# Optimization experiments

Measured on AMD Instinct MI355X. Metric: run time of the kernel, lower is better.

The kernel has to match this reference:

```python
import jax, jax.numpy as jnp
import numpy as np

B, S, H, NH = 2, 2048, 1024, 16
HD = H // NH

def setup_inputs() -> dict:
    key = jax.random.key(0)
    ks = jax.random.split(key, 11)
    scale = 1.0 / np.sqrt(H)
    inp = {
        "query": jax.random.normal(ks[0], (B, S, H), jnp.float32),
        "key": jax.random.normal(ks[1], (B, S, H), jnp.float32),
        "value": jax.random.normal(ks[2], (B, S, H), jnp.float32),
        "mask": jnp.ones((B, 1, S, S), jnp.int32),
        "Wq": jax.random.normal(ks[3], (H, H), jnp.float32) * scale,
        "bq": jnp.zeros((H,), jnp.float32),
        "Wk": jax.random.normal(ks[4], (H, H), jnp.float32) * scale,
        "bk": jnp.zeros((H,), jnp.float32),
        "Wv": jax.random.normal(ks[5], (H, H), jnp.float32) * scale,
        "bv": jnp.zeros((H,), jnp.float32),
        "Wo": jax.random.normal(ks[6], (H, H), jnp.float32) * scale,
        "bo": jnp.zeros((H,), jnp.float32),
    }
    return inp

def reference(query, key, value, mask, Wq, bq, Wk, bk, Wv, bv, Wo, bo):
    b = query.shape[0]
    # Linear projections (torch Linear: x @ W.T + b)
    Q = query @ Wq.T + bq
    K = key @ Wk.T + bk
    V = value @ Wv.T + bv
    # [b, s, h] -> [b, nh, s, hd]
    Q = Q.reshape(b, -1, NH, HD).transpose(0, 2, 1, 3)
    K = K.reshape(b, -1, NH, HD).transpose(0, 2, 1, 3)
    V = V.reshape(b, -1, NH, HD).transpose(0, 2, 1, 3)
    scores = jnp.einsum('bhid,bhjd->bhij', Q, K) / np.sqrt(HD)
    scores = jnp.where(mask == 0, jnp.float32(-1e9), scores)
    attn_weights = jax.nn.softmax(scores, axis=-1)
    # dropout = 0.0 (eval mode) -> identity
    context = jnp.einsum('bhij,bhjd->bhid', attn_weights, V)
    context = context.transpose(0, 2, 1, 3).reshape(b, -1, H)
    output = context @ Wo.T + bo
    return (output, attn_weights)
```

## Files before the change

### kernel.cpp

```cpp
#include <hip/hip_runtime.h>

#define Bq 2
#define Sq 2048
#define Hq 1024
#define NHq 16
#define HDq 64

typedef __bf16 bf16x8 __attribute__((ext_vector_type(8)));
typedef float f32x4 __attribute__((ext_vector_type(4)));

__device__ __forceinline__ unsigned short f2b(float f) {
  union { float f; unsigned int u; } v; v.f = f;
  unsigned int u = v.u;
  u += 0x7fffu + ((u >> 16) & 1);
  return (unsigned short)(u >> 16);
}

__global__ __launch_bounds__(256) void k_f2bf(const float* __restrict__ in,
                                              unsigned short* __restrict__ out, int n4) {
  int i = blockIdx.x * 256 + threadIdx.x;
  if (i >= n4) return;
  float4 v = ((const float4*)in)[i];
  ushort4 o;
  o.x = f2b(v.x); o.y = f2b(v.y); o.z = f2b(v.z); o.w = f2b(v.w);
  ((ushort4*)out)[i] = o;
}

template<int MODE>
__global__ __launch_bounds__(256) void k_gemm_bt(
    const unsigned short* __restrict__ Abase,
    const unsigned short* __restrict__ Bbase,
    const float* __restrict__ bias,
    void* __restrict__ Cout,
    int Klen, int lda, int ldb)
{
  __shared__ __align__(16) unsigned short As[128 * 32];
  __shared__ __align__(16) unsigned short Bs[128 * 32];

  const int tid = threadIdx.x;
  const int l = tid & 63;
  const int w = tid >> 6;
  const unsigned short* A  = Abase;
  const unsigned short* Bm = Bbase;
  const int row0 = blockIdx.y * 128;
  const int col0 = blockIdx.x * 128;

  const int wm = w & 1, wn = w >> 1;
  const int lrow = l & 15;
  const int lk = (l >> 4) * 8;

  f32x4 acc[4][4] = {};

  for (int kk = 0; kk < Klen; kk += 32) {
    __syncthreads();
#pragma unroll
    for (int c2 = 0; c2 < 2; ++c2) {
      int c = 2 * w + c2;
      int f = c * 512 + l * 8;
      int r = f >> 5, k = f & 31;
      __builtin_amdgcn_global_load_lds(
          (__attribute__((address_space(1))) void*)(A + (size_t)(row0 + r) * lda + kk + k),
          (__attribute__((address_space(3))) void*)(&As[c * 512]), 16, 0, 0);
      __builtin_amdgcn_global_load_lds(
          (__attribute__((address_space(1))) void*)(Bm + (size_t)(col0 + r) * ldb + kk + k),
          (__attribute__((address_space(3))) void*)(&Bs[c * 512]), 16, 0, 0);
    }
    __syncthreads();

    bf16x8 af[4], bfr[4];
#pragma unroll
    for (int mt = 0; mt < 4; ++mt)
      af[mt] = *(const bf16x8*)&As[(wm * 64 + mt * 16 + lrow) * 32 + lk];
#pragma unroll
    for (int nt = 0; nt < 4; ++nt)
      bfr[nt] = *(const bf16x8*)&Bs[(wn * 64 + nt * 16 + lrow) * 32 + lk];
#pragma unroll
    for (int mt = 0; mt < 4; ++mt)
#pragma unroll
      for (int nt = 0; nt < 4; ++nt)
        acc[mt][nt] = __builtin_amdgcn_mfma_f32_16x16x32_bf16(af[mt], bfr[nt], acc[mt][nt], 0, 0, 0);
  }

  const int quad = l >> 4;
#pragma unroll
  for (int mt = 0; mt < 4; ++mt) {
#pragma unroll
    for (int nt = 0; nt < 4; ++nt) {
#pragma unroll
      for (int r = 0; r < 4; ++r) {
        int grow = row0 + wm * 64 + mt * 16 + quad * 4 + r;
        int gcol = col0 + wn * 64 + nt * 16 + lrow;
        float v = acc[mt][nt][r];
        if constexpr (MODE == 0) {
          v += bias[gcol];
          int b = grow >> 11, s = grow & 2047;
          int nh = gcol >> 6, hd = gcol & 63;
          ((unsigned short*)Cout)[((size_t)(b * NHq + nh) * Sq + s) * HDq + hd] = f2b(v);
        } else if constexpr (MODE == 1) {
          v += bias[gcol];
          int b = grow >> 11, s = grow & 2047;
          int nh = gcol >> 6, hd = gcol & 63;
          ((unsigned short*)Cout)[((size_t)(b * NHq + nh) * HDq + hd) * Sq + s] = f2b(v);
        } else {
          ((float*)Cout)[(size_t)grow * Hq + gcol] = v + bias[gcol];
        }
      }
    }
  }
}

__global__ __launch_bounds__(256, 2) void k_attn_fused(
    const unsigned short* __restrict__ Qh,
    const unsigned short* __restrict__ Kh,
    const unsigned short* __restrict__ Vt,
    const int* __restrict__ mask,
    float* __restrict__ attn,
    unsigned short* __restrict__ ctx)
{
  __shared__ __align__(16) unsigned short Pl[64 * 16 * 32];
  __shared__ float redA[4][16];
  __shared__ float redB[4][16];

  const int tid = threadIdx.x;
  const int l = tid & 63;
  const int w = tid >> 6;
  const int row = l & 15;
  const int q = l >> 4;
  const int z = blockIdx.y;
  const int b = z >> 4, nh = z & 15;
  const int i0 = blockIdx.x * 16;

  const unsigned short* Qz = Qh + ((size_t)z * Sq + i0) * HDq;
  const unsigned short* Kz = Kh + (size_t)z * Sq * HDq;

  bf16x8 bq0 = *(const bf16x8*)&Qz[row * HDq + q * 8];
  bf16x8 bq1 = *(const bf16x8*)&Qz[row * HDq + 32 + q * 8];

  f32x4 sc[32];
#pragma unroll
  for (int t = 0; t < 32; ++t) {
    int j0 = w * 512 + t * 16;
    bf16x8 a0 = *(const bf16x8*)&Kz[(size_t)(j0 + row) * HDq + q * 8];
    bf16x8 a1 = *(const bf16x8*)&Kz[(size_t)(j0 + row) * HDq + 32 + q * 8];
    f32x4 acc = {};
    acc = __builtin_amdgcn_mfma_f32_16x16x32_bf16(a0, bq0, acc, 0, 0, 0);
    acc = __builtin_amdgcn_mfma_f32_16x16x32_bf16(a1, bq1, acc, 0, 0, 0);
    sc[t] = acc;
  }

  const int* mrow = mask + (size_t)b * Sq * Sq + (size_t)(i0 + row) * Sq;
#pragma unroll
  for (int t = 0; t < 32; ++t) {
    int j0 = w * 512 + t * 16;
    int4 mv = *(const int4*)&mrow[j0 + q * 4];
    sc[t][0] = mv.x ? sc[t][0] * 0.125f : -1e9f;
    sc[t][1] = mv.y ? sc[t][1] * 0.125f : -1e9f;
    sc[t][2] = mv.z ? sc[t][2] * 0.125f : -1e9f;
    sc[t][3] = mv.w ? sc[t][3] * 0.125f : -1e9f;
  }

  float m = -3.4e38f;
#pragma unroll
  for (int t = 0; t < 32; ++t)
    m = fmaxf(m, fmaxf(fmaxf(sc[t][0], sc[t][1]), fmaxf(sc[t][2], sc[t][3])));
  m = fmaxf(m, __shfl_xor(m, 16));
  m = fmaxf(m, __shfl_xor(m, 32));
  if (l < 16) redA[w][l] = m;
  __syncthreads();
  m = fmaxf(fmaxf(redA[0][row], redA[1][row]), fmaxf(redA[2][row], redA[3][row]));

  float s = 0.f;
#pragma unroll
  for (int t = 0; t < 32; ++t) {
#pragma unroll
    for (int r = 0; r < 4; ++r) {
      float e = __expf(sc[t][r] - m);
      sc[t][r] = e;
      s += e;
    }
  }
  s += __shfl_xor(s, 16);
  s += __shfl_xor(s, 32);
  if (l < 16) redB[w][l] = s;
  __syncthreads();
  float inv = 1.0f / (redB[0][row] + redB[1][row] + redB[2][row] + redB[3][row]);

  float* attnz = attn + (size_t)z * Sq * Sq + (size_t)(i0 + row) * Sq;
#pragma unroll
  for (int t = 0; t < 32; ++t) {
    int j0 = w * 512 + t * 16;
    float4 wv;
    wv.x = sc[t][0] * inv; wv.y = sc[t][1] * inv;
    wv.z = sc[t][2] * inv; wv.w = sc[t][3] * inv;
    *(float4*)&attnz[j0 + q * 4] = wv;
    ushort4 pb;
    pb.x = f2b(sc[t][0]); pb.y = f2b(sc[t][1]);
    pb.z = f2b(sc[t][2]); pb.w = f2b(sc[t][3]);
    int ks = j0 >> 5;
    int b5 = (j0 >> 4) & 1;
    int off = (ks * 16 + row) * 64 + (((b5 << 5) + (q << 3)) ^ ((row & 3) << 4));
    *(ushort4*)((char*)Pl + off) = pb;
  }
  __syncthreads();

  const unsigned short* Vw = Vt + (size_t)z * HDq * Sq + (size_t)(w * 16 + row) * Sq;
  f32x4 acc = {};
#pragma unroll 4
  for (int ks = 0; ks < 64; ++ks) {
    int off = (ks * 16 + row) * 64 + ((q << 4) ^ ((row & 3) << 4));
    bf16x8 af = *(const bf16x8*)((const char*)Pl + off);
    bf16x8 bf = *(const bf16x8*)&Vw[ks * 32 + q * 8];
    acc = __builtin_amdgcn_mfma_f32_16x16x32_bf16(af, bf, acc, 0, 0, 0);
  }

#pragma unroll
  for (int r = 0; r < 4; ++r) {
    int srow = i0 + q * 4 + r;
    float iv = __shfl(inv, q * 4 + r);
    ctx[((size_t)(b * Sq + srow)) * Hq + nh * HDq + w * 16 + row] = f2b(acc[r] * iv);
  }
}

extern "C" void kernel_launch(void* const* d_in, const int* in_sizes, int n_in,
                              void* d_out, int out_size, void* d_ws, size_t ws_size,
                              hipStream_t stream) {
  const float* query = (const float*)d_in[0];
  const float* key_  = (const float*)d_in[1];
  const float* value = (const float*)d_in[2];
  const int*   mask  = (const int*)d_in[3];
  const float* Wq = (const float*)d_in[4];
  const float* bq = (const float*)d_in[5];
  const float* Wk = (const float*)d_in[6];
  const float* bk = (const float*)d_in[7];
  const float* Wv = (const float*)d_in[8];
  const float* bv = (const float*)d_in[9];
  const float* Wo = (const float*)d_in[10];
  const float* bo = (const float*)d_in[11];

  unsigned short* Xq  = (unsigned short*)d_ws;
  unsigned short* Xk  = Xq  + (size_t)4096 * 1024;
  unsigned short* Xv  = Xk  + (size_t)4096 * 1024;
  unsigned short* Wqb = Xv  + (size_t)4096 * 1024;
  unsigned short* Wkb = Wqb + (size_t)1024 * 1024;
  unsigned short* Wvb = Wkb + (size_t)1024 * 1024;
  unsigned short* Wob = Wvb + (size_t)1024 * 1024;
  unsigned short* Qh  = Wob + (size_t)1024 * 1024;
  unsigned short* Kh  = Qh  + (size_t)32 * 2048 * 64;
  unsigned short* Vt  = Kh  + (size_t)32 * 2048 * 64;
  unsigned short* ctx = Vt  + (size_t)32 * 2048 * 64;

  float* outp = (float*)d_out;
  float* attn = outp + (size_t)4096 * 1024;

  k_f2bf<<<4096, 256, 0, stream>>>(query, Xq, 1048576);
  k_f2bf<<<4096, 256, 0, stream>>>(key_,  Xk, 1048576);
  k_f2bf<<<4096, 256, 0, stream>>>(value, Xv, 1048576);
  k_f2bf<<<1024, 256, 0, stream>>>(Wq, Wqb, 262144);
  k_f2bf<<<1024, 256, 0, stream>>>(Wk, Wkb, 262144);
  k_f2bf<<<1024, 256, 0, stream>>>(Wv, Wvb, 262144);
  k_f2bf<<<1024, 256, 0, stream>>>(Wo, Wob, 262144);

  dim3 gproj(8, 32, 1);
  k_gemm_bt<0><<<gproj, 256, 0, stream>>>(Xq, Wqb, bq, Qh, 1024, 1024, 1024);
  k_gemm_bt<0><<<gproj, 256, 0, stream>>>(Xk, Wkb, bk, Kh, 1024, 1024, 1024);
  k_gemm_bt<1><<<gproj, 256, 0, stream>>>(Xv, Wvb, bv, Vt, 1024, 1024, 1024);

  dim3 gattn(128, 32, 1);
  k_attn_fused<<<gattn, 256, 0, stream>>>(Qh, Kh, Vt, mask, attn, ctx);

  dim3 gout(8, 32, 1);
  k_gemm_bt<3><<<gout, 256, 0, stream>>>(ctx, Wob, bo, outp, 1024, 1024, 1024);
}
```

Measured before the change: 1.029 ms.

## Split attention block across 8 waves with split-K PV reduction and nontemporal stores

```diff
diff --git a/kernel.cpp b/kernel.cpp
--- a/kernel.cpp
+++ b/kernel.cpp
@@ -109,7 +109,7 @@
   }
 }
 
-__global__ __launch_bounds__(256, 2) void k_attn_fused(
+__global__ __launch_bounds__(512, 4) void k_attn_fused(
     const unsigned short* __restrict__ Qh,
     const unsigned short* __restrict__ Kh,
     const unsigned short* __restrict__ Vt,
@@ -118,17 +118,17 @@
     unsigned short* __restrict__ ctx)
 {
   __shared__ __align__(16) unsigned short Pl[64 * 16 * 32];
-  __shared__ float redA[4][16];
-  __shared__ float redB[4][16];
+  __shared__ float redA[8][16];
+  __shared__ float redB[8][16];
 
   const int tid = threadIdx.x;
   const int l = tid & 63;
   const int w = tid >> 6;
   const int row = l & 15;
   const int q = l >> 4;
-  const int z = blockIdx.y;
+  const int z = blockIdx.x;
   const int b = z >> 4, nh = z & 15;
-  const int i0 = blockIdx.x * 16;
+  const int i0 = blockIdx.y * 16;
 
   const unsigned short* Qz = Qh + ((size_t)z * Sq + i0) * HDq;
   const unsigned short* Kz = Kh + (size_t)z * Sq * HDq;
@@ -136,10 +136,10 @@
   bf16x8 bq0 = *(const bf16x8*)&Qz[row * HDq + q * 8];
   bf16x8 bq1 = *(const bf16x8*)&Qz[row * HDq + 32 + q * 8];
 
-  f32x4 sc[32];
-#pragma unroll
-  for (int t = 0; t < 32; ++t) {
-    int j0 = w * 512 + t * 16;
+  f32x4 sc[16];
+#pragma unroll
+  for (int t = 0; t < 16; ++t) {
+    int j0 = w * 256 + t * 16;
     bf16x8 a0 = *(const bf16x8*)&Kz[(size_t)(j0 + row) * HDq + q * 8];
     bf16x8 a1 = *(const bf16x8*)&Kz[(size_t)(j0 + row) * HDq + 32 + q * 8];
     f32x4 acc = {};
@@ -150,8 +150,8 @@
 
   const int* mrow = mask + (size_t)b * Sq * Sq + (size_t)(i0 + row) * Sq;
 #pragma unroll
-  for (int t = 0; t < 32; ++t) {
-    int j0 = w * 512 + t * 16;
+  for (int t = 0; t < 16; ++t) {
+    int j0 = w * 256 + t * 16;
     int4 mv = *(const int4*)&mrow[j0 + q * 4];
     sc[t][0] = mv.x ? sc[t][0] * 0.125f : -1e9f;
     sc[t][1] = mv.y ? sc[t][1] * 0.125f : -1e9f;
@@ -161,17 +161,18 @@
 
   float m = -3.4e38f;
 #pragma unroll
-  for (int t = 0; t < 32; ++t)
+  for (int t = 0; t < 16; ++t)
     m = fmaxf(m, fmaxf(fmaxf(sc[t][0], sc[t][1]), fmaxf(sc[t][2], sc[t][3])));
   m = fmaxf(m, __shfl_xor(m, 16));
   m = fmaxf(m, __shfl_xor(m, 32));
   if (l < 16) redA[w][l] = m;
   __syncthreads();
-  m = fmaxf(fmaxf(redA[0][row], redA[1][row]), fmaxf(redA[2][row], redA[3][row]));
+  m = fmaxf(fmaxf(fmaxf(redA[0][row], redA[1][row]), fmaxf(redA[2][row], redA[3][row])),
+            fmaxf(fmaxf(redA[4][row], redA[5][row]), fmaxf(redA[6][row], redA[7][row])));
 
   float s = 0.f;
 #pragma unroll
-  for (int t = 0; t < 32; ++t) {
+  for (int t = 0; t < 16; ++t) {
 #pragma unroll
     for (int r = 0; r < 4; ++r) {
       float e = __expf(sc[t][r] - m);
@@ -183,16 +184,17 @@
   s += __shfl_xor(s, 32);
   if (l < 16) redB[w][l] = s;
   __syncthreads();
-  float inv = 1.0f / (redB[0][row] + redB[1][row] + redB[2][row] + redB[3][row]);
+  float inv = 1.0f / (((redB[0][row] + redB[1][row]) + (redB[2][row] + redB[3][row])) +
+                      ((redB[4][row] + redB[5][row]) + (redB[6][row] + redB[7][row])));
 
   float* attnz = attn + (size_t)z * Sq * Sq + (size_t)(i0 + row) * Sq;
 #pragma unroll
-  for (int t = 0; t < 32; ++t) {
-    int j0 = w * 512 + t * 16;
-    float4 wv;
-    wv.x = sc[t][0] * inv; wv.y = sc[t][1] * inv;
-    wv.z = sc[t][2] * inv; wv.w = sc[t][3] * inv;
-    *(float4*)&attnz[j0 + q * 4] = wv;
+  for (int t = 0; t < 16; ++t) {
+    int j0 = w * 256 + t * 16;
+    f32x4 wv;
+    wv[0] = sc[t][0] * inv; wv[1] = sc[t][1] * inv;
+    wv[2] = sc[t][2] * inv; wv[3] = sc[t][3] * inv;
+    __builtin_nontemporal_store(wv, (f32x4*)&attnz[j0 + q * 4]);
     ushort4 pb;
     pb.x = f2b(sc[t][0]); pb.y = f2b(sc[t][1]);
     pb.z = f2b(sc[t][2]); pb.w = f2b(sc[t][3]);
@@ -203,21 +205,33 @@
   }
   __syncthreads();
 
-  const unsigned short* Vw = Vt + (size_t)z * HDq * Sq + (size_t)(w * 16 + row) * Sq;
+  const int jh = w >> 2, ww = w & 3;
+  const unsigned short* Vw = Vt + (size_t)z * HDq * Sq + (size_t)(ww * 16 + row) * Sq;
   f32x4 acc = {};
 #pragma unroll 4
-  for (int ks = 0; ks < 64; ++ks) {
+  for (int kss = 0; kss < 32; ++kss) {
+    int ks = jh * 32 + kss;
     int off = (ks * 16 + row) * 64 + ((q << 4) ^ ((row & 3) << 4));
     bf16x8 af = *(const bf16x8*)((const char*)Pl + off);
     bf16x8 bf = *(const bf16x8*)&Vw[ks * 32 + q * 8];
     acc = __builtin_amdgcn_mfma_f32_16x16x32_bf16(af, bf, acc, 0, 0, 0);
   }
 
-#pragma unroll
-  for (int r = 0; r < 4; ++r) {
-    int srow = i0 + q * 4 + r;
-    float iv = __shfl(inv, q * 4 + r);
-    ctx[((size_t)(b * Sq + srow)) * Hq + nh * HDq + w * 16 + row] = f2b(acc[r] * iv);
+  float* Fs = (float*)Pl;
+  __syncthreads();
+  if (jh == 0) {
+#pragma unroll
+    for (int r = 0; r < 4; ++r) Fs[ww * 256 + l * 4 + r] = acc[r];
+  }
+  __syncthreads();
+  if (jh == 1) {
+#pragma unroll
+    for (int r = 0; r < 4; ++r) {
+      float v = acc[r] + Fs[ww * 256 + l * 4 + r];
+      int srow = i0 + q * 4 + r;
+      float iv = __shfl(inv, q * 4 + r);
+      ctx[((size_t)(b * Sq + srow)) * Hq + nh * HDq + ww * 16 + row] = f2b(v * iv);
+    }
   }
 }
 
@@ -265,8 +279,8 @@
   k_gemm_bt<0><<<gproj, 256, 0, stream>>>(Xk, Wkb, bk, Kh, 1024, 1024, 1024);
   k_gemm_bt<1><<<gproj, 256, 0, stream>>>(Xv, Wvb, bv, Vt, 1024, 1024, 1024);
 
-  dim3 gattn(128, 32, 1);
-  k_attn_fused<<<gattn, 256, 0, stream>>>(Qh, Kh, Vt, mask, attn, ctx);
+  dim3 gattn(32, 128, 1);
+  k_attn_fused<<<gattn, 512, 0, stream>>>(Qh, Kh, Vt, mask, attn, ctx);
 
   dim3 gout(8, 32, 1);
   k_gemm_bt<3><<<gout, 256, 0, stream>>>(ctx, Wob, bo, outp, 1024, 1024, 1024);
```

Measured after the change: 1.057 ms. 2.6% more time.
